# Performance work log

Hardware: AMD Instinct MI355X
Metric: run time of the kernel (lower is better)

Reference implementation:

```python
import jax, jax.numpy as jnp
import numpy as np

IN_FEATURES = 4096
OUT_FEATURES = 4096
N_TOKENS = 8192


def setup_inputs() -> dict:
    key = jax.random.key(0)
    kx, kw = jax.random.split(key)
    x = jax.random.normal(kx, (N_TOKENS, IN_FEATURES), dtype=jnp.float32)
    # weight = randn(out, in) * 0.1, bias = zeros(out), per BinaryLinear.__init__
    weight = jax.random.normal(kw, (OUT_FEATURES, IN_FEATURES), dtype=jnp.float32) * 0.1
    bias = jnp.zeros((OUT_FEATURES,), dtype=jnp.float32)
    return {"x": x, "weight": weight, "bias": bias}


def reference(x, weight, bias):
    # sign-binarize weights (torch .sign(): -1/0/+1, matched by jnp.sign),
    # then dense linear: x @ sign(W)^T + b
    bin_w = jnp.sign(weight)
    return jnp.einsum('ni,oi->no', x, bin_w) + bias
```

## Files before the change

kernel.cpp:

```cpp
#include <hip/hip_runtime.h>
#include <stdint.h>

typedef __attribute__((ext_vector_type(4)))  int i32x4;
typedef __attribute__((ext_vector_type(16))) int i32x16;

#define M_TOK 8192
#define N_OUT 4096
#define K_IN  4096

#define BM 256
#define BN 256
#define BKB 64
#define NT (K_IN / BKB)
#define SLOT_BYTES 32768
#define B_OFF 16384

#define GLDS16(gp, lp)                                                         \
  __builtin_amdgcn_global_load_lds(                                            \
      (const __attribute__((address_space(1))) void*)(gp),                     \
      (__attribute__((address_space(3))) void*)(lp), 16, 0, 0)

#define VM4 asm volatile("s_waitcnt vmcnt(4)" ::: "memory")
#define VM0 asm volatile("s_waitcnt vmcnt(0)" ::: "memory")
#define NOPX ((void)0)

__global__ void __launch_bounds__(256) quant_fused(
    const float* __restrict__ x, const float* __restrict__ w,
    char* __restrict__ xq, char* __restrict__ wq, float* __restrict__ scales) {
  __shared__ float wmax[4];
  const int t = threadIdx.x;

  if (blockIdx.x < M_TOK) {
    const int row = blockIdx.x;
    const float4* rp = (const float4*)(x + (size_t)row * K_IN);

    float4 v[4];
#pragma unroll
    for (int p = 0; p < 4; p++) v[p] = rp[p * 256 + t];

    float amax = 0.f;
#pragma unroll
    for (int p = 0; p < 4; p++)
      amax = fmaxf(amax, fmaxf(fmaxf(fabsf(v[p].x), fabsf(v[p].y)),
                               fmaxf(fabsf(v[p].z), fabsf(v[p].w))));

#pragma unroll
    for (int off = 32; off > 0; off >>= 1)
      amax = fmaxf(amax, __shfl_xor(amax, off));

    if ((t & 63) == 0) wmax[t >> 6] = amax;
    __syncthreads();
    amax = fmaxf(fmaxf(wmax[0], wmax[1]), fmaxf(wmax[2], wmax[3]));
    amax = fmaxf(amax, 1e-30f);

    const float inv = 127.f / amax;
    if (t == 0) scales[row] = amax / 127.f;

    uint32_t* op = (uint32_t*)(xq + (size_t)row * K_IN);
#pragma unroll
    for (int p = 0; p < 4; p++) {
      uint32_t b0 = (uint32_t)(__float2int_rn(v[p].x * inv) & 0xFF);
      uint32_t b1 = (uint32_t)(__float2int_rn(v[p].y * inv) & 0xFF);
      uint32_t b2 = (uint32_t)(__float2int_rn(v[p].z * inv) & 0xFF);
      uint32_t b3 = (uint32_t)(__float2int_rn(v[p].w * inv) & 0xFF);
      op[p * 256 + t] = b0 | (b1 << 8) | (b2 << 16) | (b3 << 24);
    }
  } else {
    const size_t base = (size_t)(blockIdx.x - M_TOK) * 1024;
    const float4* p = (const float4*)w + base;
    uint32_t* op = (uint32_t*)wq + base;
#pragma unroll
    for (int q = 0; q < 4; q++) {
      float4 f = p[q * 256 + t];
      int s0 = (f.x > 0.f) - (f.x < 0.f);
      int s1 = (f.y > 0.f) - (f.y < 0.f);
      int s2 = (f.z > 0.f) - (f.z < 0.f);
      int s3 = (f.w > 0.f) - (f.w < 0.f);
      op[q * 256 + t] = (uint32_t)(s0 & 0xFF) | ((uint32_t)(s1 & 0xFF) << 8) |
                        ((uint32_t)(s2 & 0xFF) << 16) | ((uint32_t)(s3 & 0xFF) << 24);
    }
  }
}

__global__ void __launch_bounds__(512, 2) gemm_bin_i8(
    const char* __restrict__ A, const char* __restrict__ B,
    const float* __restrict__ scales, const float* __restrict__ bias,
    float* __restrict__ C) {
  __shared__ __align__(16) char lds[4 * SLOT_BYTES];

  const int tid  = threadIdx.x;
  const int lane = tid & 63;
  const int wv   = tid >> 6;
  const int wm   = wv >> 2;
  const int wn   = wv & 3;

  int bid = (int)blockIdx.x;
  bid = (bid & 7) * (512 >> 3) + (bid >> 3);
  const int m0 = (bid >> 4) * BM;
  const int n0 = (bid & 15) * BN;

  const int srow   = lane >> 2;
  const int schunk = (lane & 3) ^ ((lane >> 3) & 3);
  const char* gAb = A + (size_t)(m0 + wv * 32 + srow) * K_IN + schunk * 16;
  const char* gBb = B + (size_t)(n0 + wv * 32 + srow) * K_IN + schunk * 16;
  char* lAb = lds + wv * 2048;
  char* lBb = lds + B_OFF + wv * 2048;

  auto stageA = [&](int tt) {
    const size_t ko = (size_t)tt * BKB;
    char* l = lAb + (tt & 3) * SLOT_BYTES;
    GLDS16(gAb + ko, l);
    GLDS16(gAb + ko + (size_t)16 * K_IN, l + 1024);
  };
  auto stageB = [&](int tt) {
    const size_t ko = (size_t)tt * BKB;
    char* l = lBb + (tt & 3) * SLOT_BYTES;
    GLDS16(gBb + ko, l);
    GLDS16(gBb + ko + (size_t)16 * K_IN, l + 1024);
  };

  const int fr  = lane & 31;
  const int k16 = lane >> 5;
  const int x3  = (lane >> 1) & 3;
  const int aoff = wm * 8192 + fr * 64;
  const int boff = B_OFF + wn * 4096 + fr * 64;

  i32x16 acc[4][2];
#pragma unroll
  for (int m = 0; m < 4; m++)
#pragma unroll
    for (int n = 0; n < 2; n++)
#pragma unroll
      for (int r = 0; r < 16; r++) acc[m][n][r] = 0;

#define PHASE(rtile, ks, STAGE_STMT, VM_STMT)                                  \
  {                                                                            \
    const char* pA = lds + ((rtile) & 3) * SLOT_BYTES + aoff;                  \
    const char* pB = lds + ((rtile) & 3) * SLOT_BYTES + boff;                  \
    const int so = ((2 * (ks) + k16) ^ x3) << 4;                               \
    i32x4 a0 = *(const i32x4*)(pA + so);                                       \
    i32x4 a1 = *(const i32x4*)(pA + 2048 + so);                                \
    i32x4 a2 = *(const i32x4*)(pA + 4096 + so);                                \
    i32x4 a3 = *(const i32x4*)(pA + 6144 + so);                                \
    i32x4 b0 = *(const i32x4*)(pB + so);                                       \
    i32x4 b1 = *(const i32x4*)(pB + 2048 + so);                                \
    STAGE_STMT;                                                                \
    VM_STMT;                                                                   \
    __builtin_amdgcn_sched_barrier(0);                                         \
    __builtin_amdgcn_s_barrier();                                              \
    __builtin_amdgcn_sched_barrier(0);                                         \
    __builtin_amdgcn_s_setprio(1);                                             \
    acc[0][0] = __builtin_amdgcn_mfma_i32_32x32x32_i8(a0, b0, acc[0][0], 0, 0, 0); \
    acc[0][1] = __builtin_amdgcn_mfma_i32_32x32x32_i8(a0, b1, acc[0][1], 0, 0, 0); \
    acc[1][0] = __builtin_amdgcn_mfma_i32_32x32x32_i8(a1, b0, acc[1][0], 0, 0, 0); \
    acc[1][1] = __builtin_amdgcn_mfma_i32_32x32x32_i8(a1, b1, acc[1][1], 0, 0, 0); \
    acc[2][0] = __builtin_amdgcn_mfma_i32_32x32x32_i8(a2, b0, acc[2][0], 0, 0, 0); \
    acc[2][1] = __builtin_amdgcn_mfma_i32_32x32x32_i8(a2, b1, acc[2][1], 0, 0, 0); \
    acc[3][0] = __builtin_amdgcn_mfma_i32_32x32x32_i8(a3, b0, acc[3][0], 0, 0, 0); \
    acc[3][1] = __builtin_amdgcn_mfma_i32_32x32x32_i8(a3, b1, acc[3][1], 0, 0, 0); \
    __builtin_amdgcn_s_setprio(0);                                             \
    __builtin_amdgcn_sched_barrier(0);                                         \
    __builtin_amdgcn_s_barrier();                                              \
  }

  stageA(0); stageB(0); stageA(1); stageB(1);
  VM4;
  __builtin_amdgcn_sched_barrier(0);
  __builtin_amdgcn_s_barrier();
  __builtin_amdgcn_sched_barrier(0);

  for (int I = 0; I < 31; ++I) {
    const int t0 = 2 * I, t1 = t0 + 1, u0 = t0 + 2, u1 = t0 + 3;
    PHASE(t0, 0, stageA(u0), NOPX);
    PHASE(t0, 1, stageB(u0), VM4);
    PHASE(t1, 0, stageA(u1), NOPX);
    PHASE(t1, 1, stageB(u1), VM4);
  }
  PHASE(62, 0, NOPX, NOPX);
  PHASE(62, 1, NOPX, VM0);
  PHASE(63, 0, NOPX, NOPX);
  PHASE(63, 1, NOPX, NOPX);
#undef PHASE

  const int col0 = n0 + wn * 64 + (lane & 31);
  const float bv0 = bias[col0];
  const float bv1 = bias[col0 + 32];
#pragma unroll
  for (int m = 0; m < 4; m++) {
    const int rb = m0 + wm * 128 + m * 32 + ((lane >> 5) << 2);
#pragma unroll
    for (int r = 0; r < 16; r++) {
      const int row = rb + (r & 3) + ((r >> 2) << 3);
      const float sc = scales[row];
      float* cp = C + (size_t)row * N_OUT + col0;
      cp[0]  = (float)acc[m][0][r] * sc + bv0;
      cp[32] = (float)acc[m][1][r] * sc + bv1;
    }
  }
}

__global__ void fallback_gemm(const float* __restrict__ x, const float* __restrict__ w,
                              const float* __restrict__ bias, float* __restrict__ out) {
  int idx = blockIdx.x * blockDim.x + threadIdx.x;
  if (idx >= M_TOK * N_OUT) return;
  int row = idx / N_OUT, col = idx % N_OUT;
  const float* xp = x + (size_t)row * K_IN;
  const float* wp = w + (size_t)col * K_IN;
  float s = 0.f;
  for (int k = 0; k < K_IN; k++) {
    float wv = wp[k];
    float sg = wv > 0.f ? 1.f : (wv < 0.f ? -1.f : 0.f);
    s += xp[k] * sg;
  }
  out[idx] = s + bias[col];
}

extern "C" void kernel_launch(void* const* d_in, const int* in_sizes, int n_in,
                              void* d_out, int out_size, void* d_ws, size_t ws_size,
                              hipStream_t stream) {
  const float* x    = (const float*)d_in[0];
  const float* w    = (const float*)d_in[1];
  const float* bias = (const float*)d_in[2];
  float* out = (float*)d_out;

  const size_t xq_bytes = (size_t)M_TOK * K_IN;
  const size_t wq_bytes = (size_t)N_OUT * K_IN;
  const size_t sc_bytes = (size_t)M_TOK * sizeof(float);

  if (ws_size < xq_bytes + wq_bytes + sc_bytes) {
    int total = M_TOK * N_OUT;
    fallback_gemm<<<(total + 255) / 256, 256, 0, stream>>>(x, w, bias, out);
    return;
  }

  char*  xq = (char*)d_ws;
  char*  wq = (char*)d_ws + xq_bytes;
  float* sc = (float*)((char*)d_ws + xq_bytes + wq_bytes);

  quant_fused<<<M_TOK + (N_OUT * K_IN / 4) / 1024, 256, 0, stream>>>(x, w, xq, wq, sc);

  gemm_bin_i8<<<512, 512, 0, stream>>>(xq, wq, sc, bias, out);
}
```

Before: 399.3 us.

## Software-pipeline LDS fragment reads with double-buffered registers and deeper prefetch

```diff
diff --git a/kernel.cpp b/kernel.cpp
--- a/kernel.cpp
+++ b/kernel.cpp
@@ -21,7 +21,9 @@
       (__attribute__((address_space(3))) void*)(lp), 16, 0, 0)
 
 #define VM4 asm volatile("s_waitcnt vmcnt(4)" ::: "memory")
+#define VM8 asm volatile("s_waitcnt vmcnt(8)" ::: "memory")
 #define VM0 asm volatile("s_waitcnt vmcnt(0)" ::: "memory")
+#define SB0 __builtin_amdgcn_sched_barrier(0)
 #define NOPX ((void)0)
 
 __global__ void __launch_bounds__(256) quant_fused(
@@ -82,6 +84,11 @@
   }
 }
 
+struct Frags {
+  i32x4 a[2][4];
+  i32x4 b[2][2];
+};
+
 __global__ void __launch_bounds__(512, 2) gemm_bin_i8(
     const char* __restrict__ A, const char* __restrict__ B,
     const float* __restrict__ scales, const float* __restrict__ bias,
@@ -106,17 +113,14 @@
   char* lAb = lds + wv * 2048;
   char* lBb = lds + B_OFF + wv * 2048;
 
-  auto stageA = [&](int tt) {
+  auto stage = [&](int tt) {
     const size_t ko = (size_t)tt * BKB;
-    char* l = lAb + (tt & 3) * SLOT_BYTES;
-    GLDS16(gAb + ko, l);
-    GLDS16(gAb + ko + (size_t)16 * K_IN, l + 1024);
-  };
-  auto stageB = [&](int tt) {
-    const size_t ko = (size_t)tt * BKB;
-    char* l = lBb + (tt & 3) * SLOT_BYTES;
-    GLDS16(gBb + ko, l);
-    GLDS16(gBb + ko + (size_t)16 * K_IN, l + 1024);
+    char* la = lAb + (tt & 3) * SLOT_BYTES;
+    char* lb = lBb + (tt & 3) * SLOT_BYTES;
+    GLDS16(gAb + ko, la);
+    GLDS16(gAb + ko + (size_t)16 * K_IN, la + 1024);
+    GLDS16(gBb + ko, lb);
+    GLDS16(gBb + ko + (size_t)16 * K_IN, lb + 1024);
   };
 
   const int fr  = lane & 31;
@@ -124,6 +128,8 @@
   const int x3  = (lane >> 1) & 3;
   const int aoff = wm * 8192 + fr * 64;
   const int boff = B_OFF + wn * 4096 + fr * 64;
+  const int so0 = ((0 + k16) ^ x3) << 4;
+  const int so1 = ((2 + k16) ^ x3) << 4;
 
   i32x16 acc[4][2];
 #pragma unroll
@@ -133,54 +139,78 @@
 #pragma unroll
       for (int r = 0; r < 16; r++) acc[m][n][r] = 0;
 
-#define PHASE(rtile, ks, STAGE_STMT, VM_STMT)                                  \
+  Frags f0, f1;
+
+#define READF(f, tt)                                                           \
   {                                                                            \
-    const char* pA = lds + ((rtile) & 3) * SLOT_BYTES + aoff;                  \
-    const char* pB = lds + ((rtile) & 3) * SLOT_BYTES + boff;                  \
-    const int so = ((2 * (ks) + k16) ^ x3) << 4;                               \
-    i32x4 a0 = *(const i32x4*)(pA + so);                                       \
-    i32x4 a1 = *(const i32x4*)(pA + 2048 + so);                                \
-    i32x4 a2 = *(const i32x4*)(pA + 4096 + so);                                \
-    i32x4 a3 = *(const i32x4*)(pA + 6144 + so);                                \
-    i32x4 b0 = *(const i32x4*)(pB + so);                                       \
-    i32x4 b1 = *(const i32x4*)(pB + 2048 + so);                                \
+    const char* pA_ = lds + ((tt) & 3) * SLOT_BYTES + aoff;                    \
+    const char* pB_ = lds + ((tt) & 3) * SLOT_BYTES + boff;                    \
+    f.a[0][0] = *(const i32x4*)(pA_ + so0);                                    \
+    f.a[0][1] = *(const i32x4*)(pA_ + 2048 + so0);                             \
+    f.a[0][2] = *(const i32x4*)(pA_ + 4096 + so0);                             \
+    f.a[0][3] = *(const i32x4*)(pA_ + 6144 + so0);                             \
+    f.b[0][0] = *(const i32x4*)(pB_ + so0);                                    \
+    f.b[0][1] = *(const i32x4*)(pB_ + 2048 + so0);                             \
+    f.a[1][0] = *(const i32x4*)(pA_ + so1);                                    \
+    f.a[1][1] = *(const i32x4*)(pA_ + 2048 + so1);                             \
+    f.a[1][2] = *(const i32x4*)(pA_ + 4096 + so1);                             \
+    f.a[1][3] = *(const i32x4*)(pA_ + 6144 + so1);                             \
+    f.b[1][0] = *(const i32x4*)(pB_ + so1);                                    \
+    f.b[1][1] = *(const i32x4*)(pB_ + 2048 + so1);                             \
+  }
+
+#define MFMAF(f)                                                               \
+  {                                                                            \
+    __builtin_amdgcn_s_setprio(1);                                             \
+    acc[0][0] = __builtin_amdgcn_mfma_i32_32x32x32_i8(f.a[0][0], f.b[0][0], acc[0][0], 0, 0, 0); \
+    acc[0][1] = __builtin_amdgcn_mfma_i32_32x32x32_i8(f.a[0][0], f.b[0][1], acc[0][1], 0, 0, 0); \
+    acc[1][0] = __builtin_amdgcn_mfma_i32_32x32x32_i8(f.a[0][1], f.b[0][0], acc[1][0], 0, 0, 0); \
+    acc[1][1] = __builtin_amdgcn_mfma_i32_32x32x32_i8(f.a[0][1], f.b[0][1], acc[1][1], 0, 0, 0); \
+    acc[2][0] = __builtin_amdgcn_mfma_i32_32x32x32_i8(f.a[0][2], f.b[0][0], acc[2][0], 0, 0, 0); \
+    acc[2][1] = __builtin_amdgcn_mfma_i32_32x32x32_i8(f.a[0][2], f.b[0][1], acc[2][1], 0, 0, 0); \
+    acc[3][0] = __builtin_amdgcn_mfma_i32_32x32x32_i8(f.a[0][3], f.b[0][0], acc[3][0], 0, 0, 0); \
+    acc[3][1] = __builtin_amdgcn_mfma_i32_32x32x32_i8(f.a[0][3], f.b[0][1], acc[3][1], 0, 0, 0); \
+    acc[0][0] = __builtin_amdgcn_mfma_i32_32x32x32_i8(f.a[1][0], f.b[1][0], acc[0][0], 0, 0, 0); \
+    acc[0][1] = __builtin_amdgcn_mfma_i32_32x32x32_i8(f.a[1][0], f.b[1][1], acc[0][1], 0, 0, 0); \
+    acc[1][0] = __builtin_amdgcn_mfma_i32_32x32x32_i8(f.a[1][1], f.b[1][0], acc[1][0], 0, 0, 0); \
+    acc[1][1] = __builtin_amdgcn_mfma_i32_32x32x32_i8(f.a[1][1], f.b[1][1], acc[1][1], 0, 0, 0); \
+    acc[2][0] = __builtin_amdgcn_mfma_i32_32x32x32_i8(f.a[1][2], f.b[1][0], acc[2][0], 0, 0, 0); \
+    acc[2][1] = __builtin_amdgcn_mfma_i32_32x32x32_i8(f.a[1][2], f.b[1][1], acc[2][1], 0, 0, 0); \
+    acc[3][0] = __builtin_amdgcn_mfma_i32_32x32x32_i8(f.a[1][3], f.b[1][0], acc[3][0], 0, 0, 0); \
+    acc[3][1] = __builtin_amdgcn_mfma_i32_32x32x32_i8(f.a[1][3], f.b[1][1], acc[3][1], 0, 0, 0); \
+    __builtin_amdgcn_s_setprio(0);                                             \
+  }
+
+#define ITER(t_, fc, fn, STAGE_STMT, VM_STMT)                                  \
+  {                                                                            \
+    VM_STMT;                                                                   \
+    SB0;                                                                       \
+    __builtin_amdgcn_s_barrier();                                              \
+    SB0;                                                                       \
     STAGE_STMT;                                                                \
-    VM_STMT;                                                                   \
-    __builtin_amdgcn_sched_barrier(0);                                         \
-    __builtin_amdgcn_s_barrier();                                              \
-    __builtin_amdgcn_sched_barrier(0);                                         \
-    __builtin_amdgcn_s_setprio(1);                                             \
-    acc[0][0] = __builtin_amdgcn_mfma_i32_32x32x32_i8(a0, b0, acc[0][0], 0, 0, 0); \
-    acc[0][1] = __builtin_amdgcn_mfma_i32_32x32x32_i8(a0, b1, acc[0][1], 0, 0, 0); \
-    acc[1][0] = __builtin_amdgcn_mfma_i32_32x32x32_i8(a1, b0, acc[1][0], 0, 0, 0); \
-    acc[1][1] = __builtin_amdgcn_mfma_i32_32x32x32_i8(a1, b1, acc[1][1], 0, 0, 0); \
-    acc[2][0] = __builtin_amdgcn_mfma_i32_32x32x32_i8(a2, b0, acc[2][0], 0, 0, 0); \
-    acc[2][1] = __builtin_amdgcn_mfma_i32_32x32x32_i8(a2, b1, acc[2][1], 0, 0, 0); \
-    acc[3][0] = __builtin_amdgcn_mfma_i32_32x32x32_i8(a3, b0, acc[3][0], 0, 0, 0); \
-    acc[3][1] = __builtin_amdgcn_mfma_i32_32x32x32_i8(a3, b1, acc[3][1], 0, 0, 0); \
-    __builtin_amdgcn_s_setprio(0);                                             \
-    __builtin_amdgcn_sched_barrier(0);                                         \
-    __builtin_amdgcn_s_barrier();                                              \
-  }
-
-  stageA(0); stageB(0); stageA(1); stageB(1);
-  VM4;
-  __builtin_amdgcn_sched_barrier(0);
+    READF(fn, (t_) + 1);                                                       \
+    MFMAF(fc);                                                                 \
+  }
+
+  stage(0); stage(1); stage(2);
+  VM8;
+  SB0;
   __builtin_amdgcn_s_barrier();
-  __builtin_amdgcn_sched_barrier(0);
-
-  for (int I = 0; I < 31; ++I) {
-    const int t0 = 2 * I, t1 = t0 + 1, u0 = t0 + 2, u1 = t0 + 3;
-    PHASE(t0, 0, stageA(u0), NOPX);
-    PHASE(t0, 1, stageB(u0), VM4);
-    PHASE(t1, 0, stageA(u1), NOPX);
-    PHASE(t1, 1, stageB(u1), VM4);
-  }
-  PHASE(62, 0, NOPX, NOPX);
-  PHASE(62, 1, NOPX, VM0);
-  PHASE(63, 0, NOPX, NOPX);
-  PHASE(63, 1, NOPX, NOPX);
-#undef PHASE
+  SB0;
+  READF(f0, 0);
+
+  for (int I = 0; I < 30; ++I) {
+    const int t0 = 2 * I;
+    ITER(t0,     f0, f1, stage(t0 + 3), VM4);
+    ITER(t0 + 1, f1, f0, stage(t0 + 4), VM4);
+  }
+  ITER(60, f0, f1, stage(63), VM4);
+  ITER(61, f1, f0, NOPX, VM4);
+  ITER(62, f0, f1, NOPX, VM0);
+  MFMAF(f1);
+#undef ITER
+#undef MFMAF
+#undef READF
 
   const int col0 = n0 + wn * 64 + (lane & 31);
   const float bv0 = bias[col0];
```

New measurement: 397.3 us. No clear change (-0.5%).
